# Kernel tuning notes

Measured on AMD Instinct MI355X. Metric: run time of the kernel, lower is better.

Reference implementation:

```python
import jax, jax.numpy as jnp
import numpy as np

B, T, D = 1, 4096, 768
H, HD = 12, 64  # num_heads, head_dim; H*HD == D


def setup_inputs() -> dict:
    key = jax.random.key(0)
    ks = jax.random.split(key, 12)
    s = 1.0 / np.sqrt(D)  # nn.Linear-style init scale
    inp = {
        "query": jax.random.normal(ks[0], (B, T, D), jnp.float32),
        "key": jax.random.normal(ks[1], (B, T, D), jnp.float32),
        "value": jax.random.normal(ks[2], (B, T, D), jnp.float32),
        # causal mask: True positions are masked (strict upper triangle)
        "mask": jnp.triu(jnp.ones((T, T), dtype=bool), k=1),
        "Wq_w": jax.random.normal(ks[3], (D, D), jnp.float32) * s,
        "Wq_b": jax.random.normal(ks[4], (D,), jnp.float32) * s,
        "Wk_w": jax.random.normal(ks[5], (D, D), jnp.float32) * s,
        "Wk_b": jax.random.normal(ks[6], (D,), jnp.float32) * s,
        "Wv_w": jax.random.normal(ks[7], (D, D), jnp.float32) * s,
        "Wv_b": jax.random.normal(ks[8], (D,), jnp.float32) * s,
        "W0_w": jax.random.normal(ks[9], (D, D), jnp.float32) * s,
        "W0_b": jax.random.normal(ks[10], (D,), jnp.float32) * s,
    }
    return inp


def _split_heads(x):
    # (B, T, D) -> (B, H, T, HD)
    b, t, _ = x.shape
    return x.reshape(b, t, H, HD).transpose(0, 2, 1, 3)


def reference(query, key, value, mask, Wq_w, Wq_b, Wk_w, Wk_b, Wv_w, Wv_b, W0_w, W0_b):
    # Q/K/V projections (torch Linear: x @ W.T + b)
    q = _split_heads(query @ Wq_w.T + Wq_b)
    k = _split_heads(key @ Wk_w.T + Wk_b)
    v = _split_heads(value @ Wv_w.T + Wv_b)

    scale = 1.0 / jnp.sqrt(jnp.asarray(HD, q.dtype))
    scores = jnp.einsum("bhqd,bhkd->bhqk", q, k) * scale  # (B,H,T,T)
    scores = jnp.where(mask, -jnp.inf, scores)
    weights = jax.nn.softmax(scores, axis=-1)  # (B,H,T,T)
    attn = jnp.einsum("bhqk,bhkd->bhqd", weights, v)  # (B,H,T,HD)

    # concat heads: (B,H,T,HD) -> (B,T,D), then output projection
    out = attn.transpose(0, 2, 1, 3).reshape(query.shape[0], -1, D)
    output = out @ W0_w.T + W0_b
    return output, weights
```

## Files before the change

### kernel.cpp

```cpp
#include <hip/hip_runtime.h>

#define TSEQ 4096
#define DM 768
#define NHEAD 12
#define HDIM 64
#define SC 0.1803368801111204f

using f32x4  = __attribute__((ext_vector_type(4))) float;
using bf16x8 = __attribute__((ext_vector_type(8))) short;
using bf16x4 = __attribute__((ext_vector_type(4))) short;

#define LGKM_BARRIER() asm volatile("s_waitcnt lgkmcnt(0)\n\ts_barrier" ::: "memory")

__device__ __forceinline__ short f2bf(float f) {
    union { float f; unsigned u; } x; x.f = f;
    unsigned r = x.u + 0x7FFFu + ((x.u >> 16) & 1u);
    return (short)(r >> 16);
}

__device__ __forceinline__ unsigned pk2(float lo, float hi) {
    unsigned d;
    asm("v_cvt_pk_bf16_f32 %0, %1, %2" : "=v"(d) : "v"(lo), "v"(hi));
    return d;
}

__device__ __forceinline__ bf16x8 pack8(f32x4 a, f32x4 b) {
    union { unsigned u[4]; bf16x8 v; } r;
    r.u[0] = pk2(a[0], a[1]); r.u[1] = pk2(a[2], a[3]);
    r.u[2] = pk2(b[0], b[1]); r.u[3] = pk2(b[2], b[3]);
    return r.v;
}

__device__ __forceinline__ f32x4 mfma16(bf16x8 a, bf16x8 b, f32x4 c) {
    return __builtin_amdgcn_mfma_f32_16x16x32_bf16(a, b, c, 0, 0, 0);
}

__global__ __launch_bounds__(256) void gemm_qkv(
    const float* __restrict__ q_in, const float* __restrict__ k_in,
    const float* __restrict__ v_in,
    const float* __restrict__ Wq_w, const float* __restrict__ Wq_b,
    const float* __restrict__ Wk_w, const float* __restrict__ Wk_b,
    const float* __restrict__ Wv_w, const float* __restrict__ Wv_b,
    short* __restrict__ Qb, short* __restrict__ Kb, short* __restrict__ Vt)
{
    constexpr int K = DM;
    __shared__ __align__(16) short As[64 * 72];
    __shared__ __align__(16) short Bs[64 * 72];
    const int z = blockIdx.z;
    const float* A    = (z == 0) ? q_in : (z == 1) ? k_in : v_in;
    const float* W    = (z == 0) ? Wq_w : (z == 1) ? Wk_w : Wv_w;
    const float* bias = (z == 0) ? Wq_b : (z == 1) ? Wk_b : Wv_b;

    const int bm = blockIdx.x * 64;
    const int bn = blockIdx.y * 64;
    const int tid = threadIdx.x;
    const int wid = tid >> 6;
    const int lane = tid & 63;
    const int l15 = lane & 15, lq = lane >> 4;

    f32x4 acc[4] = {};
    const int sr = tid >> 3;
    const int sc = (tid & 7) * 8;

    for (int k0 = 0; k0 < K; k0 += 64) {
        #pragma unroll
        for (int it = 0; it < 2; ++it) {
            int r = sr + it * 32;
            const float* ga = A + (size_t)(bm + r) * K + k0 + sc;
            f32x4 a0 = *(const f32x4*)ga;
            f32x4 a1 = *(const f32x4*)(ga + 4);
            *(bf16x8*)&As[r * 72 + sc] = pack8(a0, a1);
            const float* gb = W + (size_t)(bn + r) * K + k0 + sc;
            f32x4 b0 = *(const f32x4*)gb;
            f32x4 b1 = *(const f32x4*)(gb + 4);
            *(bf16x8*)&Bs[r * 72 + sc] = pack8(b0, b1);
        }
        LGKM_BARRIER();
        __builtin_amdgcn_s_setprio(1);
        #pragma unroll
        for (int ks = 0; ks < 2; ++ks) {
            bf16x8 af = *(bf16x8*)&As[(wid * 16 + l15) * 72 + ks * 32 + lq * 8];
            #pragma unroll
            for (int n = 0; n < 4; ++n) {
                bf16x8 bfv = *(bf16x8*)&Bs[(n * 16 + l15) * 72 + ks * 32 + lq * 8];
                acc[n] = mfma16(af, bfv, acc[n]);
            }
        }
        __builtin_amdgcn_s_setprio(0);
        LGKM_BARRIER();
    }

    const int row0 = bm + wid * 16 + lq * 4;
    #pragma unroll
    for (int n = 0; n < 4; ++n) {
        int col = bn + n * 16 + l15;
        float b = bias[col];
        if (z == 2) {
            uint2 pv;
            pv.x = pk2(acc[n][0] + b, acc[n][1] + b);
            pv.y = pk2(acc[n][2] + b, acc[n][3] + b);
            *(uint2*)(Vt + (size_t)col * TSEQ + row0) = pv;
        } else {
            short* dst = (z == 0) ? Qb : Kb;
            #pragma unroll
            for (int r = 0; r < 4; ++r)
                dst[(size_t)(row0 + r) * DM + col] = f2bf(acc[n][r] + b);
        }
    }
}

__global__ __launch_bounds__(256) void gemm_out(
    const float* __restrict__ A, const float* __restrict__ W,
    const float* __restrict__ bias, float* __restrict__ Cout)
{
    constexpr int K = DM;
    __shared__ __align__(16) short As[64 * 72];
    __shared__ __align__(16) short Bs[64 * 72];
    const int bm = blockIdx.x * 64;
    const int bn = blockIdx.y * 64;
    const int tid = threadIdx.x;
    const int wid = tid >> 6;
    const int lane = tid & 63;
    const int l15 = lane & 15, lq = lane >> 4;

    f32x4 acc[4] = {};
    const int sr = tid >> 3;
    const int sc = (tid & 7) * 8;

    for (int k0 = 0; k0 < K; k0 += 64) {
        #pragma unroll
        for (int it = 0; it < 2; ++it) {
            int r = sr + it * 32;
            const float* ga = A + (size_t)(bm + r) * K + k0 + sc;
            f32x4 a0 = *(const f32x4*)ga;
            f32x4 a1 = *(const f32x4*)(ga + 4);
            *(bf16x8*)&As[r * 72 + sc] = pack8(a0, a1);
            const float* gb = W + (size_t)(bn + r) * K + k0 + sc;
            f32x4 b0 = *(const f32x4*)gb;
            f32x4 b1 = *(const f32x4*)(gb + 4);
            *(bf16x8*)&Bs[r * 72 + sc] = pack8(b0, b1);
        }
        LGKM_BARRIER();
        __builtin_amdgcn_s_setprio(1);
        #pragma unroll
        for (int ks = 0; ks < 2; ++ks) {
            bf16x8 af = *(bf16x8*)&As[(wid * 16 + l15) * 72 + ks * 32 + lq * 8];
            #pragma unroll
            for (int n = 0; n < 4; ++n) {
                bf16x8 bfv = *(bf16x8*)&Bs[(n * 16 + l15) * 72 + ks * 32 + lq * 8];
                acc[n] = mfma16(af, bfv, acc[n]);
            }
        }
        __builtin_amdgcn_s_setprio(0);
        LGKM_BARRIER();
    }

    const int row0 = bm + wid * 16 + lq * 4;
    #pragma unroll
    for (int n = 0; n < 4; ++n) {
        int col = bn + n * 16 + l15;
        float b = bias[col];
        #pragma unroll
        for (int r = 0; r < 4; ++r)
            Cout[(size_t)(row0 + r) * DM + col] = acc[n][r] + b;
    }
}

__global__ __launch_bounds__(256) void attn_fused(
    const short* __restrict__ Qb, const short* __restrict__ Kb,
    const short* __restrict__ Vt, float* __restrict__ Wout,
    float* __restrict__ AttnO)
{
    const int qt = 63 - blockIdx.x;
    const int h = blockIdx.y;
    const int q0 = qt * 64;
    const int tid = threadIdx.x, wid = tid >> 6, lane = tid & 63;
    const int l15 = lane & 15, lq = lane >> 4;

    __shared__ __align__(16) short lds[23040];

    const int nkt = qt + 1;

    {
        float* wbase = Wout + (size_t)h * TSEQ * TSEQ + (size_t)(q0 + wid * 16) * TSEQ;
        f32x4 z = {0.f, 0.f, 0.f, 0.f};
        for (int kt = nkt; kt < 64; ++kt) {
            #pragma unroll
            for (int i = 0; i < 4; ++i)
                __builtin_nontemporal_store(
                    z, (f32x4*)(wbase + (size_t)(lq + i * 4) * TSEQ + kt * 64 + l15 * 4));
        }
    }

    const short* qp = Qb + (size_t)(q0 + wid * 16 + l15) * DM + h * HDIM + lq * 8;
    bf16x8 qf0 = *(const bf16x8*)qp;
    bf16x8 qf1 = *(const bf16x8*)(qp + 32);

    const short* kbase = Kb + (size_t)h * HDIM;
    const short* vbase = Vt + (size_t)h * HDIM * TSEQ;
    const int myq = q0 + wid * 16 + l15;

    const int srow = tid >> 3;
    const int scol = (tid & 7) * 8;

    const int nch = (nkt + 1) >> 1;
    auto stageKbig = [&](int c, int b) {
        const int base_k = c * 128;
        const int iters = (nkt * 64 - base_k) >= 128 ? 4 : 2;
        short* dst = lds + b * (128 * 72);
        for (int it = 0; it < iters; ++it) {
            int r = srow + it * 32;
            *(bf16x8*)&dst[r * 72 + scol] =
                *(const bf16x8*)&kbase[(size_t)(base_k + r) * DM + scol];
        }
    };

    f32x4 lacc = {0.f, 0.f, 0.f, 0.f};
    stageKbig(0, 0);
    LGKM_BARRIER();
    for (int c = 0; c < nch; ++c) {
        const int b = c & 1;
        if (c + 1 < nch) stageKbig(c + 1, b ^ 1);
        const short* kb = lds + b * (128 * 72);
        #pragma unroll
        for (int t = 0; t < 2; ++t) {
            const int kt = c * 2 + t;
            if (kt >= nkt) break;
            f32x4 s[4] = {};
            __builtin_amdgcn_s_setprio(1);
            #pragma unroll
            for (int ks = 0; ks < 2; ++ks) {
                bf16x8 qf = ks ? qf1 : qf0;
                #pragma unroll
                for (int n = 0; n < 4; ++n) {
                    bf16x8 kf = *(const bf16x8*)
                        &kb[(t * 64 + n * 16 + l15) * 72 + ks * 32 + lq * 8];
                    s[n] = mfma16(kf, qf, s[n]);
                }
            }
            __builtin_amdgcn_s_setprio(0);
            if (kt == qt) {
                #pragma unroll
                for (int n = 0; n < 4; ++n) {
                    int kb0 = kt * 64 + n * 16 + lq * 4;
                    #pragma unroll
                    for (int r = 0; r < 4; ++r)
                        lacc[n] += (kb0 + r <= myq) ? exp2f(s[n][r] * SC) : 0.f;
                }
            } else {
                #pragma unroll
                for (int n = 0; n < 4; ++n)
                    #pragma unroll
                    for (int r = 0; r < 4; ++r)
                        lacc[n] += exp2f(s[n][r] * SC);
            }
        }
        LGKM_BARRIER();
    }
    float lsum = (lacc[0] + lacc[1]) + (lacc[2] + lacc[3]);
    lsum += __shfl_xor(lsum, 16);
    lsum += __shfl_xor(lsum, 32);
    const float nlog = -__log2f(lsum);

    short* Ks2 = lds;
    short* Vs2 = lds + 2 * 64 * 72;
    short* Psw = lds + 4 * 64 * 72 + wid * (16 * 72);

    bf16x8 krg0, krg1, vrg0, vrg1;
    auto loadKV = [&](int kt) {
        krg0 = *(const bf16x8*)&kbase[(size_t)(kt * 64 + srow) * DM + scol];
        krg1 = *(const bf16x8*)&kbase[(size_t)(kt * 64 + srow + 32) * DM + scol];
        vrg0 = *(const bf16x8*)&vbase[(size_t)srow * TSEQ + kt * 64 + scol];
        vrg1 = *(const bf16x8*)&vbase[(size_t)(srow + 32) * TSEQ + kt * 64 + scol];
    };
    auto writeKV = [&](int b) {
        short* kd = Ks2 + b * (64 * 72);
        short* vd = Vs2 + b * (64 * 72);
        *(bf16x8*)&kd[srow * 72 + scol] = krg0;
        *(bf16x8*)&kd[(srow + 32) * 72 + scol] = krg1;
        *(bf16x8*)&vd[srow * 72 + scol] = vrg0;
        *(bf16x8*)&vd[(srow + 32) * 72 + scol] = vrg1;
    };

    float* wq = Wout + (size_t)h * TSEQ * TSEQ + (size_t)myq * TSEQ;
    f32x4 o[4] = {};
    loadKV(0);
    writeKV(0);
    LGKM_BARRIER();
    for (int kt = 0; kt < nkt; ++kt) {
        const int b = kt & 1;
        const bool more = (kt + 1 < nkt);
        if (more) {
            loadKV(kt + 1);
            __builtin_amdgcn_sched_barrier(0);
        }
        f32x4 s[4] = {};
        __builtin_amdgcn_s_setprio(1);
        #pragma unroll
        for (int ks = 0; ks < 2; ++ks) {
            bf16x8 qf = ks ? qf1 : qf0;
            #pragma unroll
            for (int n = 0; n < 4; ++n) {
                bf16x8 kf = *(const bf16x8*)
                    &Ks2[b * (64 * 72) + (n * 16 + l15) * 72 + ks * 32 + lq * 8];
                s[n] = mfma16(kf, qf, s[n]);
            }
        }
        __builtin_amdgcn_s_setprio(0);
        const bool diag = (kt == qt);
        #pragma unroll
        for (int n = 0; n < 4; ++n) {
            const int kb0 = kt * 64 + n * 16 + lq * 4;
            f32x4 p;
            #pragma unroll
            for (int r = 0; r < 4; ++r) {
                float e = exp2f(fmaf(s[n][r], SC, nlog));
                p[r] = (diag && (kb0 + r > myq)) ? 0.f : e;
            }
            *(f32x4*)(wq + kb0) = p;
            uint2 pv;
            pv.x = pk2(p[0], p[1]);
            pv.y = pk2(p[2], p[3]);
            *(uint2*)&Psw[l15 * 72 + n * 16 + lq * 4] = pv;
        }
        __builtin_amdgcn_s_setprio(1);
        #pragma unroll
        for (int ks = 0; ks < 2; ++ks) {
            bf16x8 pf = *(bf16x8*)&Psw[l15 * 72 + ks * 32 + lq * 8];
            #pragma unroll
            for (int n = 0; n < 4; ++n) {
                bf16x8 vf = *(const bf16x8*)
                    &Vs2[b * (64 * 72) + (n * 16 + l15) * 72 + ks * 32 + lq * 8];
                o[n] = mfma16(pf, vf, o[n]);
            }
        }
        __builtin_amdgcn_s_setprio(0);
        if (more) {
            __builtin_amdgcn_sched_barrier(0);
            writeKV(b ^ 1);
        }
        LGKM_BARRIER();
    }

    #pragma unroll
    for (int n = 0; n < 4; ++n) {
        int col = h * HDIM + n * 16 + l15;
        #pragma unroll
        for (int r = 0; r < 4; ++r) {
            int row = q0 + wid * 16 + lq * 4 + r;
            AttnO[(size_t)row * DM + col] = o[n][r];
        }
    }
}

extern "C" void kernel_launch(void* const* d_in, const int* in_sizes, int n_in,
                              void* d_out, int out_size, void* d_ws, size_t ws_size,
                              hipStream_t stream)
{
    const float* q_in = (const float*)d_in[0];
    const float* k_in = (const float*)d_in[1];
    const float* v_in = (const float*)d_in[2];
    const float* Wq_w = (const float*)d_in[4];
    const float* Wq_b = (const float*)d_in[5];
    const float* Wk_w = (const float*)d_in[6];
    const float* Wk_b = (const float*)d_in[7];
    const float* Wv_w = (const float*)d_in[8];
    const float* Wv_b = (const float*)d_in[9];
    const float* W0_w = (const float*)d_in[10];
    const float* W0_b = (const float*)d_in[11];

    float* out  = (float*)d_out;
    float* wout = out + (size_t)TSEQ * DM;

    short* Qb = (short*)d_ws;
    short* Kb = Qb + (size_t)TSEQ * DM;
    short* Vt = Kb + (size_t)TSEQ * DM;
    float* AttnO = (float*)(Vt + (size_t)TSEQ * DM);

    gemm_qkv<<<dim3(TSEQ / 64, DM / 64, 3), 256, 0, stream>>>(
        q_in, k_in, v_in, Wq_w, Wq_b, Wk_w, Wk_b, Wv_w, Wv_b, Qb, Kb, Vt);
    attn_fused<<<dim3(64, NHEAD), 256, 0, stream>>>(Qb, Kb, Vt, wout, AttnO);
    gemm_out<<<dim3(TSEQ / 64, DM / 64), 256, 0, stream>>>(AttnO, W0_w, W0_b, out);
}
```

Before: 335.3 us.

## Enlarge GEMM tiles to 64x256 with 512 threads and XCD-aware block remap

Both projection GEMMs move from 64x64 tiles with 256 threads to 64x256 tiles with 512 threads. Each wave now computes a 32x64 sub-tile, so every A fragment is reused across more MFMAs and fewer blocks re-read the activation rows. A 1D grid with a swizzled block index is meant to place blocks that share a row panel on the same XCD for L2 reuse. The cost is fewer blocks (576 and 192), which may leave CUs idle in gemm_out, plus more LDS per block. Attention, which is most of the runtime, is unchanged.

```diff
diff --git a/kernel.cpp b/kernel.cpp
--- a/kernel.cpp
+++ b/kernel.cpp
@@ -35,7 +35,7 @@
     return __builtin_amdgcn_mfma_f32_16x16x32_bf16(a, b, c, 0, 0, 0);
 }
 
-__global__ __launch_bounds__(256) void gemm_qkv(
+__global__ __launch_bounds__(512) void gemm_qkv(
     const float* __restrict__ q_in, const float* __restrict__ k_in,
     const float* __restrict__ v_in,
     const float* __restrict__ Wq_w, const float* __restrict__ Wq_b,
@@ -45,124 +45,145 @@
 {
     constexpr int K = DM;
     __shared__ __align__(16) short As[64 * 72];
-    __shared__ __align__(16) short Bs[64 * 72];
-    const int z = blockIdx.z;
+    __shared__ __align__(16) short Bs[256 * 72];
+
+    const int D = blockIdx.x;
+    const int o = (D & 7) * 72 + (D >> 3);
+    const int bm = (o & 63) * 64;
+    const int g  = o >> 6;
+    const int bn = (g % 3) * 256;
+    const int z  = g / 3;
+
     const float* A    = (z == 0) ? q_in : (z == 1) ? k_in : v_in;
     const float* W    = (z == 0) ? Wq_w : (z == 1) ? Wk_w : Wv_w;
     const float* bias = (z == 0) ? Wq_b : (z == 1) ? Wk_b : Wv_b;
 
-    const int bm = blockIdx.x * 64;
-    const int bn = blockIdx.y * 64;
     const int tid = threadIdx.x;
     const int wid = tid >> 6;
     const int lane = tid & 63;
+    const int wm = wid >> 2, wn = wid & 3;
     const int l15 = lane & 15, lq = lane >> 4;
 
-    f32x4 acc[4] = {};
+    f32x4 acc[2][4] = {};
     const int sr = tid >> 3;
     const int sc = (tid & 7) * 8;
 
     for (int k0 = 0; k0 < K; k0 += 64) {
-        #pragma unroll
-        for (int it = 0; it < 2; ++it) {
-            int r = sr + it * 32;
-            const float* ga = A + (size_t)(bm + r) * K + k0 + sc;
-            f32x4 a0 = *(const f32x4*)ga;
-            f32x4 a1 = *(const f32x4*)(ga + 4);
-            *(bf16x8*)&As[r * 72 + sc] = pack8(a0, a1);
+        {
+            const float* ga = A + (size_t)(bm + sr) * K + k0 + sc;
+            *(bf16x8*)&As[sr * 72 + sc] =
+                pack8(*(const f32x4*)ga, *(const f32x4*)(ga + 4));
+        }
+        #pragma unroll
+        for (int it = 0; it < 4; ++it) {
+            int r = sr + it * 64;
             const float* gb = W + (size_t)(bn + r) * K + k0 + sc;
-            f32x4 b0 = *(const f32x4*)gb;
-            f32x4 b1 = *(const f32x4*)(gb + 4);
-            *(bf16x8*)&Bs[r * 72 + sc] = pack8(b0, b1);
+            *(bf16x8*)&Bs[r * 72 + sc] =
+                pack8(*(const f32x4*)gb, *(const f32x4*)(gb + 4));
         }
         LGKM_BARRIER();
         __builtin_amdgcn_s_setprio(1);
         #pragma unroll
         for (int ks = 0; ks < 2; ++ks) {
-            bf16x8 af = *(bf16x8*)&As[(wid * 16 + l15) * 72 + ks * 32 + lq * 8];
+            bf16x8 af0 = *(bf16x8*)&As[(wm * 32 + l15) * 72 + ks * 32 + lq * 8];
+            bf16x8 af1 = *(bf16x8*)&As[(wm * 32 + 16 + l15) * 72 + ks * 32 + lq * 8];
             #pragma unroll
             for (int n = 0; n < 4; ++n) {
-                bf16x8 bfv = *(bf16x8*)&Bs[(n * 16 + l15) * 72 + ks * 32 + lq * 8];
-                acc[n] = mfma16(af, bfv, acc[n]);
+                bf16x8 bfv = *(bf16x8*)&Bs[(wn * 64 + n * 16 + l15) * 72 + ks * 32 + lq * 8];
+                acc[0][n] = mfma16(af0, bfv, acc[0][n]);
+                acc[1][n] = mfma16(af1, bfv, acc[1][n]);
             }
         }
         __builtin_amdgcn_s_setprio(0);
         LGKM_BARRIER();
     }
 
-    const int row0 = bm + wid * 16 + lq * 4;
     #pragma unroll
-    for (int n = 0; n < 4; ++n) {
-        int col = bn + n * 16 + l15;
-        float b = bias[col];
-        if (z == 2) {
-            uint2 pv;
-            pv.x = pk2(acc[n][0] + b, acc[n][1] + b);
-            pv.y = pk2(acc[n][2] + b, acc[n][3] + b);
-            *(uint2*)(Vt + (size_t)col * TSEQ + row0) = pv;
-        } else {
-            short* dst = (z == 0) ? Qb : Kb;
-            #pragma unroll
-            for (int r = 0; r < 4; ++r)
-                dst[(size_t)(row0 + r) * DM + col] = f2bf(acc[n][r] + b);
-        }
-    }
-}
-
-__global__ __launch_bounds__(256) void gemm_out(
+    for (int mf = 0; mf < 2; ++mf) {
+        const int row0 = bm + wm * 32 + mf * 16 + lq * 4;
+        #pragma unroll
+        for (int n = 0; n < 4; ++n) {
+            int col = bn + wn * 64 + n * 16 + l15;
+            float b = bias[col];
+            if (z == 2) {
+                uint2 pv;
+                pv.x = pk2(acc[mf][n][0] + b, acc[mf][n][1] + b);
+                pv.y = pk2(acc[mf][n][2] + b, acc[mf][n][3] + b);
+                *(uint2*)(Vt + (size_t)col * TSEQ + row0) = pv;
+            } else {
+                short* dst = (z == 0) ? Qb : Kb;
+                #pragma unroll
+                for (int r = 0; r < 4; ++r)
+                    dst[(size_t)(row0 + r) * DM + col] = f2bf(acc[mf][n][r] + b);
+            }
+        }
+    }
+}
+
+__global__ __launch_bounds__(512) void gemm_out(
     const float* __restrict__ A, const float* __restrict__ W,
     const float* __restrict__ bias, float* __restrict__ Cout)
 {
     constexpr int K = DM;
     __shared__ __align__(16) short As[64 * 72];
-    __shared__ __align__(16) short Bs[64 * 72];
-    const int bm = blockIdx.x * 64;
-    const int bn = blockIdx.y * 64;
+    __shared__ __align__(16) short Bs[256 * 72];
+
+    const int D = blockIdx.x;
+    const int o = (D & 7) * 24 + (D >> 3);
+    const int bm = (o & 63) * 64;
+    const int bn = (o >> 6) * 256;
+
     const int tid = threadIdx.x;
     const int wid = tid >> 6;
     const int lane = tid & 63;
+    const int wm = wid >> 2, wn = wid & 3;
     const int l15 = lane & 15, lq = lane >> 4;
 
-    f32x4 acc[4] = {};
+    f32x4 acc[2][4] = {};
     const int sr = tid >> 3;
     const int sc = (tid & 7) * 8;
 
     for (int k0 = 0; k0 < K; k0 += 64) {
-        #pragma unroll
-        for (int it = 0; it < 2; ++it) {
-            int r = sr + it * 32;
-            const float* ga = A + (size_t)(bm + r) * K + k0 + sc;
-            f32x4 a0 = *(const f32x4*)ga;
-            f32x4 a1 = *(const f32x4*)(ga + 4);
-            *(bf16x8*)&As[r * 72 + sc] = pack8(a0, a1);
+        {
+            const float* ga = A + (size_t)(bm + sr) * K + k0 + sc;
+            *(bf16x8*)&As[sr * 72 + sc] =
+                pack8(*(const f32x4*)ga, *(const f32x4*)(ga + 4));
+        }
+        #pragma unroll
+        for (int it = 0; it < 4; ++it) {
+            int r = sr + it * 64;
             const float* gb = W + (size_t)(bn + r) * K + k0 + sc;
-            f32x4 b0 = *(const f32x4*)gb;
-            f32x4 b1 = *(const f32x4*)(gb + 4);
-            *(bf16x8*)&Bs[r * 72 + sc] = pack8(b0, b1);
+            *(bf16x8*)&Bs[r * 72 + sc] =
+                pack8(*(const f32x4*)gb, *(const f32x4*)(gb + 4));
         }
         LGKM_BARRIER();
         __builtin_amdgcn_s_setprio(1);
         #pragma unroll
         for (int ks = 0; ks < 2; ++ks) {
-            bf16x8 af = *(bf16x8*)&As[(wid * 16 + l15) * 72 + ks * 32 + lq * 8];
+            bf16x8 af0 = *(bf16x8*)&As[(wm * 32 + l15) * 72 + ks * 32 + lq * 8];
+            bf16x8 af1 = *(bf16x8*)&As[(wm * 32 + 16 + l15) * 72 + ks * 32 + lq * 8];
             #pragma unroll
             for (int n = 0; n < 4; ++n) {
-                bf16x8 bfv = *(bf16x8*)&Bs[(n * 16 + l15) * 72 + ks * 32 + lq * 8];
-                acc[n] = mfma16(af, bfv, acc[n]);
+                bf16x8 bfv = *(bf16x8*)&Bs[(wn * 64 + n * 16 + l15) * 72 + ks * 32 + lq * 8];
+                acc[0][n] = mfma16(af0, bfv, acc[0][n]);
+                acc[1][n] = mfma16(af1, bfv, acc[1][n]);
             }
         }
         __builtin_amdgcn_s_setprio(0);
         LGKM_BARRIER();
     }
 
-    const int row0 = bm + wid * 16 + lq * 4;
     #pragma unroll
-    for (int n = 0; n < 4; ++n) {
-        int col = bn + n * 16 + l15;
-        float b = bias[col];
-        #pragma unroll
-        for (int r = 0; r < 4; ++r)
-            Cout[(size_t)(row0 + r) * DM + col] = acc[n][r] + b;
+    for (int mf = 0; mf < 2; ++mf) {
+        const int row0 = bm + wm * 32 + mf * 16 + lq * 4;
+        #pragma unroll
+        for (int n = 0; n < 4; ++n) {
+            int col = bn + wn * 64 + n * 16 + l15;
+            float b = bias[col];
+            #pragma unroll
+            for (int r = 0; r < 4; ++r)
+                Cout[(size_t)(row0 + r) * DM + col] = acc[mf][n][r] + b;
+        }
     }
 }
 
@@ -377,8 +398,8 @@
     short* Vt = Kb + (size_t)TSEQ * DM;
     float* AttnO = (float*)(Vt + (size_t)TSEQ * DM);
 
-    gemm_qkv<<<dim3(TSEQ / 64, DM / 64, 3), 256, 0, stream>>>(
+    gemm_qkv<<<576, 512, 0, stream>>>(
         q_in, k_in, v_in, Wq_w, Wq_b, Wk_w, Wk_b, Wv_w, Wv_b, Qb, Kb, Vt);
     attn_fused<<<dim3(64, NHEAD), 256, 0, stream>>>(Qb, Kb, Vt, wout, AttnO);
-    gemm_out<<<dim3(TSEQ / 64, DM / 64), 256, 0, stream>>>(AttnO, W0_w, W0_b, out);
-}
+    gemm_out<<<192, 512, 0, stream>>>(AttnO, W0_w, W0_b, out);
+}
```

Result: faster. 319.1 us (-4.8%).
